# Performance work log

Hardware: AMD Instinct MI355X
Metric: run time of the kernel (lower is better)

## Reference

```python
import jax, jax.numpy as jnp
import numpy as np

CONF_THRESHOLD = 0.25
IOU_THRESHOLD = 0.45
NUM_CLASSES = 18
TOPK = 300  # fixed candidate budget per class (jit-compatible replacement for boolean masking)


def setup_inputs() -> dict:
    key = jax.random.key(0)
    # raw head output [B, 4+num_classes, N_anchors]; wrapper permutes to [B, N, C]
    out = jax.random.normal(key, (32, 4 + NUM_CLASSES, 8400), dtype=jnp.float32)
    return {"out": out}


def _pairwise_iou(boxes):
    # boxes: [K, 4] in xyxy
    x1, y1, x2, y2 = boxes[:, 0], boxes[:, 1], boxes[:, 2], boxes[:, 3]
    area = jnp.clip(x2 - x1, 0.0) * jnp.clip(y2 - y1, 0.0)  # [K]
    ix1 = jnp.maximum(x1[:, None], x1[None, :])
    iy1 = jnp.maximum(y1[:, None], y1[None, :])
    ix2 = jnp.minimum(x2[:, None], x2[None, :])
    iy2 = jnp.minimum(y2[:, None], y2[None, :])
    inter = jnp.clip(ix2 - ix1, 0.0) * jnp.clip(iy2 - iy1, 0.0)  # [K, K]
    union = area[:, None] + area[None, :] - inter
    return inter / jnp.maximum(union, 1e-9)


def _nms_one_class(boxes_xyxy, class_scores):
    # boxes_xyxy: [N, 4], class_scores: [N]
    # conf-threshold masking -> fixed-size top-k candidate set (scores sorted desc)
    masked = jnp.where(class_scores > CONF_THRESHOLD, class_scores, -1.0)
    vals, idx = jax.lax.top_k(masked, TOPK)          # [K], [K]
    cboxes = boxes_xyxy[idx]                          # [K, 4]
    cvalid = vals > CONF_THRESHOLD                    # [K]
    iou = _pairwise_iou(cboxes)                       # [K, K]
    rng = jnp.arange(TOPK)

    # greedy NMS over score-sorted candidates: box i (if kept) suppresses later
    # boxes with IoU > threshold -- identical to torchvision.ops.nms semantics
    def body(i, keep):
        sup = (iou[i] > IOU_THRESHOLD) & keep[i] & (rng > i)
        return keep & ~sup

    keep = jax.lax.fori_loop(0, TOPK, body, cvalid)
    return cboxes, vals, keep


def reference(out):
    x = out.transpose(0, 2, 1)                        # [B, N, 4+nc]
    raw_boxes = x[..., :4]
    scores = jax.nn.sigmoid(x[..., 4:])               # [B, N, nc]
    cx, cy, w, h = raw_boxes[..., 0], raw_boxes[..., 1], raw_boxes[..., 2], raw_boxes[..., 3]
    boxes_xyxy = jnp.stack([cx - w / 2, cy - h / 2, cx + w / 2, cy + h / 2], axis=-1)  # [B, N, 4]

    def per_image(bx, sc):
        # vmap the per-class NMS loop (classes on axis 1 of sc)
        cboxes, vals, keep = jax.vmap(_nms_one_class, in_axes=(None, 1))(bx, sc)  # [nc, K, ...]
        cls_ids = jnp.broadcast_to(
            jnp.arange(NUM_CLASSES, dtype=bx.dtype)[:, None], (NUM_CLASSES, TOPK)
        )
        det = jnp.concatenate([cboxes, vals[..., None], cls_ids[..., None]], axis=-1)  # [nc, K, 6]
        det = det * keep[..., None].astype(det.dtype)  # zero out suppressed / below-conf rows
        return det.reshape(NUM_CLASSES * TOPK, 6)

    # [B, nc*K, 6]; fixed-shape padded equivalent of the variable-length detection lists
    return jax.vmap(per_image)(boxes_xyxy, scores)
```

## Files before the change

### kernel.cpp

```cpp
#include <hip/hip_runtime.h>
#include <cstdint>

#pragma clang fp contract(off)

#define NB      32
#define NC      18
#define NA      8400
#define NCH     (4 + NC)
#define NTASK   (NB * NC)
#define TOPK    300
#define TARGET  316
#define NBINS   2048
#define CAP     1024
#define CONF    0.25f
#define IOU_T   0.45f
#define NT      512
#define NW      (NT / 64)
#define PREF_X  1.4f
#define XHI     (-1.0984f)
#define XLO     (-1.0988f)

#define FAST_KBASE 0xBFB00000u
#define FAST_SHIFT 14
#define FB_KBASE   0x40000000u
#define FB_SHIFT   21

#define M45 (30198989.0 / 67108864.0)

typedef unsigned long long ull;

__device__ __forceinline__ float sigmoidf(float x) {
    return 1.0f / (1.0f + expf(-x));
}
__device__ __forceinline__ unsigned int mono_key(unsigned int bits) {
    return (bits & 0x80000000u) ? ~bits : (bits | 0x80000000u);
}
__device__ __forceinline__ unsigned int mono_inv(unsigned int key) {
    return (key & 0x80000000u) ? (key ^ 0x80000000u) : ~key;
}
__device__ __forceinline__ bool conf_pass(float x) {
    if (x >= XHI) return true;
    if (x <= XLO) return false;
    return sigmoidf(x) > CONF;
}
__device__ __forceinline__ unsigned int make_key(float x) {
    return conf_pass(x) ? mono_key(__float_as_uint(x)) : 0u;
}
__device__ __forceinline__ ull readlane64(ull v, int i) {
    unsigned lo = (unsigned)__builtin_amdgcn_readlane((int)(unsigned)(v & 0xFFFFFFFFull), i);
    unsigned hi = (unsigned)__builtin_amdgcn_readlane((int)(unsigned)(v >> 32), i);
    return ((ull)hi << 32) | (ull)lo;
}

__device__ __forceinline__ void suffix_find(unsigned int* hist, unsigned int* wtot,
                                            int target, int tid, int* s_T1) {
    const int base = tid * (NBINS / NT);
    unsigned int v = 0;
#pragma unroll
    for (int k = 0; k < NBINS / NT; ++k) v += hist[base + k];
    const int lane = tid & 63;
    unsigned int s = v;
#pragma unroll
    for (int d = 1; d < 64; d <<= 1) {
        unsigned int o = __shfl_down(s, d, 64);
        if (lane + d < 64) s += o;
    }
    if (lane == 0) wtot[tid >> 6] = s;
    __syncthreads();
    unsigned int above_waves = 0;
    for (int wv = (tid >> 6) + 1; wv < NW; ++wv) above_waves += wtot[wv];
    unsigned int acc = (s - v) + above_waves;
    for (int bin = base + (NBINS / NT) - 1; bin >= base; --bin) {
        unsigned int cnt = hist[bin];
        if (acc < (unsigned int)target && acc + cnt >= (unsigned int)target) *s_T1 = bin;
        acc += cnt;
    }
    __syncthreads();
}

#define OFF_CAND   8192
#define POOL1_BYTES 16384

#define PIN64(x) asm volatile("" : "+v"(x))

__global__ __launch_bounds__(NT, 4) void k_fused(const float* __restrict__ in,
                                                 float* __restrict__ out) {
    __shared__ __align__(16) unsigned char pool[POOL1_BYTES];
    __shared__ __align__(16) float4 sBox[TOPK];
    __shared__ float sVal[TOPK];
    __shared__ float sAr[TOPK];
    __shared__ unsigned int wtot[NW];
    __shared__ unsigned short actIdx[TOPK];
    __shared__ unsigned short sPos[TOPK];
    __shared__ ull s_remC[5];
    __shared__ unsigned int s_cnt, s_cnt2, s_nAct;
    __shared__ int s_T1;

    unsigned int* hist = (unsigned int*)pool;
    ull* cand2 = (ull*)pool;
    ull* cand  = (ull*)(pool + OFF_CAND);
    ull* sSup  = (ull*)pool;

    const int tid = threadIdx.x;
    const int lane = tid & 63;
    const int wave = tid >> 6;
    const ull ltm = (1ull << lane) - 1ull;
    const int t = blockIdx.x;
    const int b = (t & 7) + 8 * ((t >> 3) & 3);
    const int c = t >> 5;
    const float* cls = in + (size_t)b * NCH * NA + (size_t)(4 + c) * NA;
    const float* box = in + (size_t)b * NCH * NA;

    for (int i = tid; i < NBINS; i += NT) hist[i] = 0;
    for (int r = tid; r < TOPK; r += NT) {
        sBox[r] = float4{0.f, 0.f, 0.f, 0.f};
        sVal[r] = 0.f;
        sAr[r] = 0.f;
    }
    if (tid == 0) { s_cnt = 0; s_cnt2 = 0; s_T1 = -1; }
    __syncthreads();

    {
        const float4* cls4 = (const float4*)cls;
        int q = tid;
        float4 v = cls4[q];
        while (true) {
            const int qn = q + NT;
            const bool more = qn < NA / 4;
            float4 vn;
            if (more) vn = cls4[qn];

            const unsigned int i0 = (unsigned int)q * 4u;
            float xs[4] = {v.x, v.y, v.z, v.w};
            ull m[4];
            unsigned int cnt = 0;
#pragma unroll
            for (int u = 0; u < 4; ++u) {
                m[u] = __ballot(xs[u] > PREF_X);
                cnt += (unsigned int)__popcll(m[u]);
            }
            if (cnt) {
                unsigned int base = 0;
                if (lane == 0) base = atomicAdd(&s_cnt, cnt);
                base = (unsigned int)__builtin_amdgcn_readfirstlane((int)base);
                unsigned int pre = 0;
#pragma unroll
                for (int u = 0; u < 4; ++u) {
                    if (xs[u] > PREF_X) {
                        unsigned int mk = mono_key(__float_as_uint(xs[u]));
                        atomicAdd(&hist[min((mk - FAST_KBASE) >> FAST_SHIFT,
                                            (unsigned)(NBINS - 1))], 1u);
                        unsigned int p = base + pre + (unsigned int)__popcll(m[u] & ltm);
                        if (p < CAP)
                            cand[p] = ((ull)mk << 32) | (ull)(~(i0 + u));
                    }
                    pre += (unsigned int)__popcll(m[u]);
                }
            }
            if (!more) break;
            v = vn; q = qn;
        }
    }
    __syncthreads();

    const int pcnt = (int)s_cnt;
    if (pcnt >= TARGET && pcnt <= CAP) {
        suffix_find(hist, wtot, TARGET, tid, &s_T1);
        const ull thr = ((ull)FAST_KBASE + ((ull)(unsigned int)s_T1 << FAST_SHIFT)) << 32;
        const int iters = (pcnt + NT - 1) / NT;
        for (int it = 0; it < iters; ++it) {
            int e = tid + it * NT;
            bool act = e < pcnt;
            ull k = act ? cand[e] : 0ull;
            bool sel = act && (k >= thr);
            ull mb = __ballot(sel);
            unsigned int cnt = (unsigned int)__popcll(mb);
            if (cnt) {
                unsigned int basep = 0;
                if (lane == 0) basep = atomicAdd(&s_cnt2, cnt);
                basep = (unsigned int)__builtin_amdgcn_readfirstlane((int)basep);
                if (sel) {
                    float xv = __uint_as_float(mono_inv((unsigned int)(k >> 32)));
                    float sv = sigmoidf(xv);
                    unsigned int p = basep + (unsigned int)__popcll(mb & ltm);
                    if (p < CAP)
                        cand2[p] = ((ull)__float_as_uint(sv) << 32) | (k & 0xFFFFFFFFull);
                }
            }
        }
        __syncthreads();
    } else {
        __syncthreads();
        for (int i = tid; i < NBINS; i += NT) hist[i] = 0;
        __syncthreads();
        {
            const float4* cls4 = (const float4*)cls;
            for (int q = tid; q < NA / 4; q += NT) {
                float4 v = cls4[q];
                unsigned int kx = make_key(v.x), ky = make_key(v.y);
                unsigned int kz = make_key(v.z), kw = make_key(v.w);
                if (kx) atomicAdd(&hist[min((kx - FB_KBASE) >> FB_SHIFT, (unsigned)(NBINS - 1))], 1u);
                if (ky) atomicAdd(&hist[min((ky - FB_KBASE) >> FB_SHIFT, (unsigned)(NBINS - 1))], 1u);
                if (kz) atomicAdd(&hist[min((kz - FB_KBASE) >> FB_SHIFT, (unsigned)(NBINS - 1))], 1u);
                if (kw) atomicAdd(&hist[min((kw - FB_KBASE) >> FB_SHIFT, (unsigned)(NBINS - 1))], 1u);
            }
        }
        __syncthreads();
        suffix_find(hist, wtot, TARGET, tid, &s_T1);
        {
            const ull thr = (s_T1 < 0) ? 0ull
                : ((ull)FB_KBASE + ((ull)(unsigned int)s_T1 << FB_SHIFT));
            const float4* cls4 = (const float4*)cls;
            for (int q = tid; q < NA / 4; q += NT) {
                float4 v = cls4[q];
                const unsigned int i0 = (unsigned int)q * 4u;
                float xs[4] = {v.x, v.y, v.z, v.w};
#pragma unroll
                for (int u = 0; u < 4; ++u) {
                    unsigned int d = make_key(xs[u]);
                    if (d && (ull)d >= thr) {
                        unsigned int p = atomicAdd(&s_cnt2, 1u);
                        if (p < CAP) {
                            float sv = sigmoidf(xs[u]);
                            cand2[p] = ((ull)__float_as_uint(sv) << 32) | (ull)(~(i0 + u));
                        }
                    }
                }
            }
        }
        __syncthreads();
    }

    const int F = min((int)s_cnt2, CAP);
    const int numSel = min(F, TOPK);

    for (int e = tid; e < F; e += NT) {
        ull k = cand2[e];
        unsigned int i = ~(unsigned int)(k & 0xFFFFFFFFull);
        float cx = box[i];
        float cy = box[NA + i];
        float w  = box[2 * NA + i];
        float h  = box[3 * NA + i];
        int rank = 0;
        int o = 0;
#pragma unroll 2
        for (; o + 4 <= F; o += 4) {
            ulonglong2 p0 = *(const ulonglong2*)&cand2[o];
            ulonglong2 p1 = *(const ulonglong2*)&cand2[o + 2];
            rank += (p0.x > k) + (p0.y > k) + (p1.x > k) + (p1.y > k);
        }
        for (; o < F; ++o) rank += (cand2[o] > k) ? 1 : 0;
        if (rank < TOPK) {
            float hw = w * 0.5f, hh = h * 0.5f;
            float x1 = cx - hw, y1 = cy - hh, x2 = cx + hw, y2 = cy + hh;
            sBox[rank] = float4{x1, y1, x2, y2};
            sVal[rank] = __uint_as_float((unsigned int)(k >> 32));
            sAr[rank] = fmaxf(x2 - x1, 0.f) * fmaxf(y2 - y1, 0.f);
        }
    }
    __syncthreads();

    for (int i = tid; i < TOPK * 5; i += NT) sSup[i] = 0ull;
    {
        int r = tid;
        bool act = (r < TOPK) && (r < numSel) && (sAr[r] > 0.0f);
        ull mb = __ballot(act);
        if (lane == 0) wtot[wave] = (unsigned int)__popcll(mb);
        __syncthreads();
        unsigned int basew = 0;
        for (int w2 = 0; w2 < wave; ++w2) basew += wtot[w2];
        if (tid == 0) {
            unsigned int tot = 0;
            for (int w2 = 0; w2 < NW; ++w2) tot += wtot[w2];
            s_nAct = tot;
        }
        if (act) {
            unsigned int p = basew + (unsigned int)__popcll(mb & ltm);
            actIdx[p] = (unsigned short)r;
            sPos[r] = (unsigned short)p;
        }
    }
    __syncthreads();
    const int nAct = (int)s_nAct;

    {
        float4 cb[5];
        float ca[5];
#pragma unroll
        for (int w = 0; w < 5; ++w) {
            int jc = (w << 6) + lane;
            bool v = jc < nAct;
            int j = v ? (int)actIdx[jc] : 0;
            cb[w] = v ? sBox[j] : float4{0.f, 0.f, 0.f, 0.f};
            ca[w] = v ? sAr[j] : 0.f;
        }
        const int wlast = (nAct > 0) ? ((nAct - 1) >> 6) : -1;
        for (int p = wave; p < nAct; p += NW) {
            int r = actIdx[p];
            float4 bi = sBox[r];
            float ai = sAr[r];
            const int w0 = p >> 6;
#pragma unroll
            for (int w = 0; w < 5; ++w) {
                if (w >= w0 && w <= wlast) {
                    const int jc = (w << 6) + lane;
                    bool supb = false;
                    if (jc < nAct && jc > p) {
                        float xx1 = fmaxf(bi.x, cb[w].x);
                        float yy1 = fmaxf(bi.y, cb[w].y);
                        float xx2 = fminf(bi.z, cb[w].z);
                        float yy2 = fminf(bi.w, cb[w].w);
                        float iw = fmaxf(xx2 - xx1, 0.0f);
                        float ih = fmaxf(yy2 - yy1, 0.0f);
                        float inter = iw * ih;
                        float un = ai + ca[w] - inter;
                        float D = fmaxf(un, 1e-9f);
                        supb = (double)inter > M45 * (double)D;
                    }
                    ull bal = __ballot(supb);
                    if (lane == 0) sSup[p * 5 + w] = bal;
                }
            }
        }
    }
    __syncthreads();

    if (wave == 0) {
        ull rem0 = 0, rem1 = 0, rem2 = 0, rem3 = 0, rem4 = 0;
        {
            const ull* p = sSup + (size_t)lane * 5;
            ull B0 = p[0], B1 = p[1], B2 = p[2], B3 = p[3], B4 = p[4];
            PIN64(B0); PIN64(B1); PIN64(B2); PIN64(B3); PIN64(B4);
            ull nz = __ballot((B0 | B1 | B2 | B3 | B4) != 0ull);
            while (nz) {
                int i = __builtin_ctzll(nz);
                nz &= nz - 1;
                if (!((rem0 >> i) & 1ull)) {
                    rem0 |= readlane64(B0, i); rem1 |= readlane64(B1, i);
                    rem2 |= readlane64(B2, i); rem3 |= readlane64(B3, i);
                    rem4 |= readlane64(B4, i);
                }
            }
        }
        if (nAct > 64) {
            const ull* p = sSup + (size_t)(64 + lane) * 5;
            ull B0 = p[0], B1 = p[1], B2 = p[2], B3 = p[3], B4 = p[4];
            PIN64(B0); PIN64(B1); PIN64(B2); PIN64(B3); PIN64(B4);
            ull nz = __ballot((B0 | B1 | B2 | B3 | B4) != 0ull);
            while (nz) {
                int i = __builtin_ctzll(nz);
                nz &= nz - 1;
                if (!((rem1 >> i) & 1ull)) {
                    rem0 |= readlane64(B0, i); rem1 |= readlane64(B1, i);
                    rem2 |= readlane64(B2, i); rem3 |= readlane64(B3, i);
                    rem4 |= readlane64(B4, i);
                }
            }
        }
        if (nAct > 128) {
            const ull* p = sSup + (size_t)(128 + lane) * 5;
            ull B0 = p[0], B1 = p[1], B2 = p[2], B3 = p[3], B4 = p[4];
            PIN64(B0); PIN64(B1); PIN64(B2); PIN64(B3); PIN64(B4);
            ull nz = __ballot((B0 | B1 | B2 | B3 | B4) != 0ull);
            while (nz) {
                int i = __builtin_ctzll(nz);
                nz &= nz - 1;
                if (!((rem2 >> i) & 1ull)) {
                    rem0 |= readlane64(B0, i); rem1 |= readlane64(B1, i);
                    rem2 |= readlane64(B2, i); rem3 |= readlane64(B3, i);
                    rem4 |= readlane64(B4, i);
                }
            }
        }
        if (nAct > 192) {
            const ull* p = sSup + (size_t)(192 + lane) * 5;
            ull B0 = p[0], B1 = p[1], B2 = p[2], B3 = p[3], B4 = p[4];
            PIN64(B0); PIN64(B1); PIN64(B2); PIN64(B3); PIN64(B4);
            ull nz = __ballot((B0 | B1 | B2 | B3 | B4) != 0ull);
            while (nz) {
                int i = __builtin_ctzll(nz);
                nz &= nz - 1;
                if (!((rem3 >> i) & 1ull)) {
                    rem0 |= readlane64(B0, i); rem1 |= readlane64(B1, i);
                    rem2 |= readlane64(B2, i); rem3 |= readlane64(B3, i);
                    rem4 |= readlane64(B4, i);
                }
            }
        }
        if (nAct > 256) {
            const bool v4 = lane < (TOPK - 256);
            const ull* p = sSup + (size_t)(256 + (v4 ? lane : 0)) * 5;
            ull B0 = v4 ? p[0] : 0ull, B1 = v4 ? p[1] : 0ull, B2 = v4 ? p[2] : 0ull,
                B3 = v4 ? p[3] : 0ull, B4 = v4 ? p[4] : 0ull;
            PIN64(B0); PIN64(B1); PIN64(B2); PIN64(B3); PIN64(B4);
            ull nz = __ballot((B0 | B1 | B2 | B3 | B4) != 0ull);
            while (nz) {
                int i = __builtin_ctzll(nz);
                nz &= nz - 1;
                if (!((rem4 >> i) & 1ull)) {
                    rem0 |= readlane64(B0, i); rem1 |= readlane64(B1, i);
                    rem2 |= readlane64(B2, i); rem3 |= readlane64(B3, i);
                    rem4 |= readlane64(B4, i);
                }
            }
        }
        if (lane == 0) {
            s_remC[0] = rem0; s_remC[1] = rem1; s_remC[2] = rem2;
            s_remC[3] = rem3; s_remC[4] = rem4;
        }
    }
    __syncthreads();

    {
        const int r = tid;
        if (r < TOPK) {
            float x1 = 0.f, y1 = 0.f, x2 = 0.f, y2 = 0.f, vv = 0.f, cc = 0.f;
            if (r < numSel) {
                bool sup = false;
                if (sAr[r] > 0.0f) {
                    int p = (int)sPos[r];
                    sup = (s_remC[p >> 6] >> (p & 63)) & 1ull;
                }
                if (!sup) {
                    float4 bb = sBox[r];
                    x1 = bb.x; y1 = bb.y; x2 = bb.z; y2 = bb.w;
                    vv = sVal[r]; cc = (float)c;
                }
            }
            float* outp = out + ((size_t)b * NC + c) * (TOPK * 6);
            float* row = outp + r * 6;
            *(float2*)(row)     = float2{x1, y1};
            *(float2*)(row + 2) = float2{x2, y2};
            *(float2*)(row + 4) = float2{vv, cc};
        }
    }
}

extern "C" void kernel_launch(void* const* d_in, const int* in_sizes, int n_in,
                              void* d_out, int out_size, void* d_ws, size_t ws_size,
                              hipStream_t stream) {
    const float* in = (const float*)d_in[0];
    float* out = (float*)d_out;
    (void)d_ws; (void)ws_size;

    k_fused<<<NTASK, NT, 0, stream>>>(in, out);
}
```

Before: 86.28 us.

## Replace candidate rank-counting with histogram bucket sort on sigmoid keys

The fast path now computes the sigmoid during the first scan and bins candidates by sigmoid bits. It records each candidate's slot within its bin, then builds a suffix-sum prefix over the bins. Candidates are scattered into bucket-sorted order, and each one's rank is its bin offset plus a small count within the bin. This replaces the O(F^2) all-pairs rank counting and the separate compaction pass, and deepens the load prefetch to two iterations. The cost is extra shared memory (a prefix array and a slot array), which may lower occupancy. The zero-initialisation of sBox/sVal/sAr is also dropped, which relies on the fast path always filling all TOPK ranks.

```diff
diff --git a/kernel.cpp b/kernel.cpp
--- a/kernel.cpp
+++ b/kernel.cpp
@@ -20,8 +20,8 @@
 #define XHI     (-1.0984f)
 #define XLO     (-1.0988f)
 
-#define FAST_KBASE 0xBFB00000u
-#define FAST_SHIFT 14
+#define SV_KBASE 0x3F4D0000u
+#define SV_SHIFT 11
 #define FB_KBASE   0x40000000u
 #define FB_SHIFT   21
 
@@ -34,9 +34,6 @@
 }
 __device__ __forceinline__ unsigned int mono_key(unsigned int bits) {
     return (bits & 0x80000000u) ? ~bits : (bits | 0x80000000u);
-}
-__device__ __forceinline__ unsigned int mono_inv(unsigned int key) {
-    return (key & 0x80000000u) ? (key ^ 0x80000000u) : ~key;
 }
 __device__ __forceinline__ bool conf_pass(float x) {
     if (x >= XHI) return true;
@@ -89,6 +86,8 @@
     __shared__ __align__(16) float4 sBox[TOPK];
     __shared__ float sVal[TOPK];
     __shared__ float sAr[TOPK];
+    __shared__ unsigned int S[NBINS];
+    __shared__ unsigned short slotArr[CAP];
     __shared__ unsigned int wtot[NW];
     __shared__ unsigned short actIdx[TOPK];
     __shared__ unsigned short sPos[TOPK];
@@ -97,9 +96,10 @@
     __shared__ int s_T1;
 
     unsigned int* hist = (unsigned int*)pool;
-    ull* cand2 = (ull*)pool;
-    ull* cand  = (ull*)(pool + OFF_CAND);
-    ull* sSup  = (ull*)pool;
+    ull* cand   = (ull*)(pool + OFF_CAND);
+    ull* sorted = (ull*)(pool + OFF_CAND);
+    ull* cand2  = (ull*)pool;
+    ull* sSup   = (ull*)pool;
 
     const int tid = threadIdx.x;
     const int lane = tid & 63;
@@ -111,81 +111,131 @@
     const float* cls = in + (size_t)b * NCH * NA + (size_t)(4 + c) * NA;
     const float* box = in + (size_t)b * NCH * NA;
 
+    const float4* cls4 = (const float4*)cls;
+    float4 v  = cls4[tid];
+    float4 vn = cls4[tid + NT];
+
     for (int i = tid; i < NBINS; i += NT) hist[i] = 0;
-    for (int r = tid; r < TOPK; r += NT) {
-        sBox[r] = float4{0.f, 0.f, 0.f, 0.f};
-        sVal[r] = 0.f;
-        sAr[r] = 0.f;
-    }
     if (tid == 0) { s_cnt = 0; s_cnt2 = 0; s_T1 = -1; }
     __syncthreads();
 
-    {
-        const float4* cls4 = (const float4*)cls;
-        int q = tid;
-        float4 v = cls4[q];
-        while (true) {
-            const int qn = q + NT;
-            const bool more = qn < NA / 4;
-            float4 vn;
-            if (more) vn = cls4[qn];
-
-            const unsigned int i0 = (unsigned int)q * 4u;
-            float xs[4] = {v.x, v.y, v.z, v.w};
-            ull m[4];
-            unsigned int cnt = 0;
+    for (int q = tid; q < NA / 4; q += NT) {
+        const int qpp = q + 2 * NT;
+        float4 vf;
+        const bool havef = qpp < NA / 4;
+        if (havef) vf = cls4[qpp];
+
+        const unsigned int i0 = (unsigned int)q * 4u;
+        float xs[4] = {v.x, v.y, v.z, v.w};
+        ull m[4];
+        unsigned int cnt = 0;
+#pragma unroll
+        for (int u = 0; u < 4; ++u) {
+            m[u] = __ballot(xs[u] > PREF_X);
+            cnt += (unsigned int)__popcll(m[u]);
+        }
+        if (cnt) {
+            unsigned int base = 0;
+            if (lane == 0) base = atomicAdd(&s_cnt, cnt);
+            base = (unsigned int)__builtin_amdgcn_readfirstlane((int)base);
+            unsigned int pre = 0;
 #pragma unroll
             for (int u = 0; u < 4; ++u) {
-                m[u] = __ballot(xs[u] > PREF_X);
-                cnt += (unsigned int)__popcll(m[u]);
-            }
-            if (cnt) {
-                unsigned int base = 0;
-                if (lane == 0) base = atomicAdd(&s_cnt, cnt);
-                base = (unsigned int)__builtin_amdgcn_readfirstlane((int)base);
-                unsigned int pre = 0;
-#pragma unroll
-                for (int u = 0; u < 4; ++u) {
-                    if (xs[u] > PREF_X) {
-                        unsigned int mk = mono_key(__float_as_uint(xs[u]));
-                        atomicAdd(&hist[min((mk - FAST_KBASE) >> FAST_SHIFT,
-                                            (unsigned)(NBINS - 1))], 1u);
-                        unsigned int p = base + pre + (unsigned int)__popcll(m[u] & ltm);
-                        if (p < CAP)
-                            cand[p] = ((ull)mk << 32) | (ull)(~(i0 + u));
+                if (xs[u] > PREF_X) {
+                    float sv = sigmoidf(xs[u]);
+                    unsigned int svb = __float_as_uint(sv);
+                    unsigned int bin = min((svb - SV_KBASE) >> SV_SHIFT,
+                                           (unsigned)(NBINS - 1));
+                    unsigned int slot = atomicAdd(&hist[bin], 1u);
+                    unsigned int p = base + pre + (unsigned int)__popcll(m[u] & ltm);
+                    if (p < CAP) {
+                        cand[p] = ((ull)svb << 32) | (ull)(~(i0 + u));
+                        slotArr[p] = (unsigned short)slot;
                     }
-                    pre += (unsigned int)__popcll(m[u]);
-                }
-            }
-            if (!more) break;
-            v = vn; q = qn;
-        }
+                }
+                pre += (unsigned int)__popcll(m[u]);
+            }
+        }
+        v = vn; vn = vf;
     }
     __syncthreads();
 
     const int pcnt = (int)s_cnt;
+    int numSel;
     if (pcnt >= TARGET && pcnt <= CAP) {
-        suffix_find(hist, wtot, TARGET, tid, &s_T1);
-        const ull thr = ((ull)FAST_KBASE + ((ull)(unsigned int)s_T1 << FAST_SHIFT)) << 32;
-        const int iters = (pcnt + NT - 1) / NT;
-        for (int it = 0; it < iters; ++it) {
-            int e = tid + it * NT;
-            bool act = e < pcnt;
-            ull k = act ? cand[e] : 0ull;
-            bool sel = act && (k >= thr);
-            ull mb = __ballot(sel);
-            unsigned int cnt = (unsigned int)__popcll(mb);
-            if (cnt) {
-                unsigned int basep = 0;
-                if (lane == 0) basep = atomicAdd(&s_cnt2, cnt);
-                basep = (unsigned int)__builtin_amdgcn_readfirstlane((int)basep);
-                if (sel) {
-                    float xv = __uint_as_float(mono_inv((unsigned int)(k >> 32)));
-                    float sv = sigmoidf(xv);
-                    unsigned int p = basep + (unsigned int)__popcll(mb & ltm);
-                    if (p < CAP)
-                        cand2[p] = ((ull)__float_as_uint(sv) << 32) | (k & 0xFFFFFFFFull);
-                }
+        numSel = TOPK;
+
+        {
+            const int basebin = tid * (NBINS / NT);
+            unsigned int cs[NBINS / NT];
+            unsigned int vsum = 0;
+#pragma unroll
+            for (int k = 0; k < NBINS / NT; ++k) { cs[k] = hist[basebin + k]; vsum += cs[k]; }
+            unsigned int s = vsum;
+#pragma unroll
+            for (int d = 1; d < 64; d <<= 1) {
+                unsigned int o = __shfl_down(s, d, 64);
+                if (lane + d < 64) s += o;
+            }
+            if (lane == 0) wtot[wave] = s;
+            __syncthreads();
+            unsigned int above = 0;
+            for (int w2 = wave + 1; w2 < NW; ++w2) above += wtot[w2];
+            unsigned int acc = (s - vsum) + above;
+#pragma unroll
+            for (int k = NBINS / NT - 1; k >= 0; --k) { S[basebin + k] = acc; acc += cs[k]; }
+        }
+        __syncthreads();
+
+        ull k0 = 0, k1 = 0;
+        unsigned int pos0 = 0, pos1 = 0, g0 = 0, g1 = 0, c0 = 0, c1 = 0;
+        const bool a0 = tid < pcnt, a1 = tid + NT < pcnt;
+        float cx0 = 0.f, cy0 = 0.f, w0 = 0.f, h0 = 0.f;
+        float cx1 = 0.f, cy1 = 0.f, w1 = 0.f, h1 = 0.f;
+        if (a0) {
+            k0 = cand[tid];
+            unsigned int svb = (unsigned int)(k0 >> 32);
+            unsigned int bin = min((svb - SV_KBASE) >> SV_SHIFT, (unsigned)(NBINS - 1));
+            g0 = S[bin]; c0 = hist[bin];
+            pos0 = g0 + (unsigned int)slotArr[tid];
+            unsigned int i = ~(unsigned int)(k0 & 0xFFFFFFFFull);
+            cx0 = box[i]; cy0 = box[NA + i]; w0 = box[2 * NA + i]; h0 = box[3 * NA + i];
+        }
+        if (a1) {
+            k1 = cand[tid + NT];
+            unsigned int svb = (unsigned int)(k1 >> 32);
+            unsigned int bin = min((svb - SV_KBASE) >> SV_SHIFT, (unsigned)(NBINS - 1));
+            g1 = S[bin]; c1 = hist[bin];
+            pos1 = g1 + (unsigned int)slotArr[tid + NT];
+            unsigned int i = ~(unsigned int)(k1 & 0xFFFFFFFFull);
+            cx1 = box[i]; cy1 = box[NA + i]; w1 = box[2 * NA + i]; h1 = box[3 * NA + i];
+        }
+        __syncthreads();
+
+        if (a0) sorted[pos0] = k0;
+        if (a1) sorted[pos1] = k1;
+        __syncthreads();
+
+        if (a0) {
+            int rank = (int)g0;
+            for (unsigned int j = g0; j < g0 + c0; ++j) rank += (sorted[j] > k0) ? 1 : 0;
+            if (rank < TOPK) {
+                float hw = w0 * 0.5f, hh = h0 * 0.5f;
+                float x1 = cx0 - hw, y1 = cy0 - hh, x2 = cx0 + hw, y2 = cy0 + hh;
+                sBox[rank] = float4{x1, y1, x2, y2};
+                sVal[rank] = __uint_as_float((unsigned int)(k0 >> 32));
+                sAr[rank] = fmaxf(x2 - x1, 0.f) * fmaxf(y2 - y1, 0.f);
+            }
+        }
+        if (a1) {
+            int rank = (int)g1;
+            for (unsigned int j = g1; j < g1 + c1; ++j) rank += (sorted[j] > k1) ? 1 : 0;
+            if (rank < TOPK) {
+                float hw = w1 * 0.5f, hh = h1 * 0.5f;
+                float x1 = cx1 - hw, y1 = cy1 - hh, x2 = cx1 + hw, y2 = cy1 + hh;
+                sBox[rank] = float4{x1, y1, x2, y2};
+                sVal[rank] = __uint_as_float((unsigned int)(k1 >> 32));
+                sAr[rank] = fmaxf(x2 - x1, 0.f) * fmaxf(y2 - y1, 0.f);
             }
         }
         __syncthreads();
@@ -194,11 +244,10 @@
         for (int i = tid; i < NBINS; i += NT) hist[i] = 0;
         __syncthreads();
         {
-            const float4* cls4 = (const float4*)cls;
             for (int q = tid; q < NA / 4; q += NT) {
-                float4 v = cls4[q];
-                unsigned int kx = make_key(v.x), ky = make_key(v.y);
-                unsigned int kz = make_key(v.z), kw = make_key(v.w);
+                float4 vq = cls4[q];
+                unsigned int kx = make_key(vq.x), ky = make_key(vq.y);
+                unsigned int kz = make_key(vq.z), kw = make_key(vq.w);
                 if (kx) atomicAdd(&hist[min((kx - FB_KBASE) >> FB_SHIFT, (unsigned)(NBINS - 1))], 1u);
                 if (ky) atomicAdd(&hist[min((ky - FB_KBASE) >> FB_SHIFT, (unsigned)(NBINS - 1))], 1u);
                 if (kz) atomicAdd(&hist[min((kz - FB_KBASE) >> FB_SHIFT, (unsigned)(NBINS - 1))], 1u);
@@ -210,11 +259,10 @@
         {
             const ull thr = (s_T1 < 0) ? 0ull
                 : ((ull)FB_KBASE + ((ull)(unsigned int)s_T1 << FB_SHIFT));
-            const float4* cls4 = (const float4*)cls;
             for (int q = tid; q < NA / 4; q += NT) {
-                float4 v = cls4[q];
+                float4 vq = cls4[q];
                 const unsigned int i0 = (unsigned int)q * 4u;
-                float xs[4] = {v.x, v.y, v.z, v.w};
+                float xs[4] = {vq.x, vq.y, vq.z, vq.w};
 #pragma unroll
                 for (int u = 0; u < 4; ++u) {
                     unsigned int d = make_key(xs[u]);
@@ -229,36 +277,34 @@
             }
         }
         __syncthreads();
-    }
-
-    const int F = min((int)s_cnt2, CAP);
-    const int numSel = min(F, TOPK);
-
-    for (int e = tid; e < F; e += NT) {
-        ull k = cand2[e];
-        unsigned int i = ~(unsigned int)(k & 0xFFFFFFFFull);
-        float cx = box[i];
-        float cy = box[NA + i];
-        float w  = box[2 * NA + i];
-        float h  = box[3 * NA + i];
-        int rank = 0;
-        int o = 0;
+        const int F = min((int)s_cnt2, CAP);
+        numSel = min(F, TOPK);
+        for (int e = tid; e < F; e += NT) {
+            ull k = cand2[e];
+            unsigned int i = ~(unsigned int)(k & 0xFFFFFFFFull);
+            float cx = box[i];
+            float cy = box[NA + i];
+            float w  = box[2 * NA + i];
+            float h  = box[3 * NA + i];
+            int rank = 0;
+            int o = 0;
 #pragma unroll 2
-        for (; o + 4 <= F; o += 4) {
-            ulonglong2 p0 = *(const ulonglong2*)&cand2[o];
-            ulonglong2 p1 = *(const ulonglong2*)&cand2[o + 2];
-            rank += (p0.x > k) + (p0.y > k) + (p1.x > k) + (p1.y > k);
-        }
-        for (; o < F; ++o) rank += (cand2[o] > k) ? 1 : 0;
-        if (rank < TOPK) {
-            float hw = w * 0.5f, hh = h * 0.5f;
-            float x1 = cx - hw, y1 = cy - hh, x2 = cx + hw, y2 = cy + hh;
-            sBox[rank] = float4{x1, y1, x2, y2};
-            sVal[rank] = __uint_as_float((unsigned int)(k >> 32));
-            sAr[rank] = fmaxf(x2 - x1, 0.f) * fmaxf(y2 - y1, 0.f);
-        }
-    }
-    __syncthreads();
+            for (; o + 4 <= F; o += 4) {
+                ulonglong2 p0 = *(const ulonglong2*)&cand2[o];
+                ulonglong2 p1 = *(const ulonglong2*)&cand2[o + 2];
+                rank += (p0.x > k) + (p0.y > k) + (p1.x > k) + (p1.y > k);
+            }
+            for (; o < F; ++o) rank += (cand2[o] > k) ? 1 : 0;
+            if (rank < TOPK) {
+                float hw = w * 0.5f, hh = h * 0.5f;
+                float x1 = cx - hw, y1 = cy - hh, x2 = cx + hw, y2 = cy + hh;
+                sBox[rank] = float4{x1, y1, x2, y2};
+                sVal[rank] = __uint_as_float((unsigned int)(k >> 32));
+                sAr[rank] = fmaxf(x2 - x1, 0.f) * fmaxf(y2 - y1, 0.f);
+            }
+        }
+        __syncthreads();
+    }
 
     for (int i = tid; i < TOPK * 5; i += NT) sSup[i] = 0ull;
     {
@@ -289,10 +335,10 @@
 #pragma unroll
         for (int w = 0; w < 5; ++w) {
             int jc = (w << 6) + lane;
-            bool v = jc < nAct;
-            int j = v ? (int)actIdx[jc] : 0;
-            cb[w] = v ? sBox[j] : float4{0.f, 0.f, 0.f, 0.f};
-            ca[w] = v ? sAr[j] : 0.f;
+            bool vv = jc < nAct;
+            int j = vv ? (int)actIdx[jc] : 0;
+            cb[w] = vv ? sBox[j] : float4{0.f, 0.f, 0.f, 0.f};
+            ca[w] = vv ? sAr[j] : 0.f;
         }
         const int wlast = (nAct > 0) ? ((nAct - 1) >> 6) : -1;
         for (int p = wave; p < nAct; p += NW) {
```

After: 82.66 us. 1.04x faster.
